# Performance work log

Measured on AMD Instinct MI355X. Metric: run time of the kernel, lower is better.

Reference implementation:

```python
import jax, jax.numpy as jnp
import numpy as np
from jax import lax

# Module constants (from init_kwargs)
B, C = 2, 64            # batch, in_channel
H, W, D = 64, 64, 64    # size
GROUPS = 2


def setup_inputs() -> dict:
    key = jax.random.key(0)
    ks = jax.random.split(key, 4)
    x = jax.random.normal(ks[0], (B, H * W * D, C), dtype=jnp.float32)
    # TransverseConv: Conv3d(2, W*2, (H,3,3), pad (0,1,1)) -> weight (O,I,kD,kH,kW)
    w_t = jax.random.normal(ks[1], (W * GROUPS, GROUPS, H, 3, 3), dtype=jnp.float32) * 0.02
    b_t = jnp.zeros((W * GROUPS,), jnp.float32)
    # CoronalConv: Conv3d(2, W*2, (3,3,D), pad (1,1,0))
    w_c = jax.random.normal(ks[2], (W * GROUPS, GROUPS, 3, 3, D), dtype=jnp.float32) * 0.02
    b_c = jnp.zeros((W * GROUPS,), jnp.float32)
    # map: Conv3d(2C, C, 1) stored as dense (C, 2C)
    w_map = jax.random.normal(ks[3], (C, 2 * C), dtype=jnp.float32) * 0.02
    b_map = jnp.zeros((C,), jnp.float32)
    return {"x": x, "w_t": w_t, "b_t": b_t, "w_c": w_c, "b_c": b_c,
            "w_map": w_map, "b_map": b_map}


def _forward(x, w_t, b_t, w_c, b_c, w_map, b_map):
    Bx, N, Cx = x.shape
    xg = x.transpose(0, 2, 1).reshape(Bx, Cx, H, W, D)   # (B,C,H,W,D)
    shortcut = xg
    xr = xg.reshape(Bx * Cx // GROUPS, GROUPS, H, W, D)
    dn = ('NCDHW', 'OIDHW', 'NCDHW')
    # Transverse: kernel spans full H -> output (B*C/2, 2W, 1, W, D)
    tans = lax.conv_general_dilated(xr, w_t, (1, 1, 1), [(0, 0), (1, 1), (1, 1)],
                                    dimension_numbers=dn)
    tans = tans + b_t[None, :, None, None, None]
    tans = tans.reshape(Bx, Cx, W, W, D)                 # (B,C,W,W,D)
    # Coronal: kernel spans full D -> output (B*C/2, 2W, H, W, 1)
    cor = lax.conv_general_dilated(xr, w_c, (1, 1, 1), [(1, 1), (1, 1), (0, 0)],
                                   dimension_numbers=dn)
    cor = cor + b_c[None, :, None, None, None]
    cor = cor.reshape(Bx, Cx, W, H, W)                   # (B,C,W,H,W)
    t1 = tans.transpose(0, 1, 3, 2, 4)                   # (B,C,W,W,D)
    c1 = cor.transpose(0, 1, 4, 3, 2)                    # (B,C,W,H,W)
    f = jnp.matmul(c1, t1).transpose(0, 1, 3, 2, 4)      # (B,C,H,W,D)
    attn = jnp.matmul(cor, tans).transpose(0, 1, 3, 2, 4)  # (B,C,H,W,D)
    cat = jnp.concatenate([shortcut * f, attn], axis=1)  # (B,2C,H,W,D)
    mapped = jnp.einsum('bkhwd,ck->bchwd', cat, w_map) + b_map[None, :, None, None, None]
    out = jax.nn.gelu(mapped, approximate=False)         # torch nn.GELU = exact erf
    return out.reshape(Bx, Cx, -1).transpose(0, 2, 1)    # (B,N,C)


def reference(x, w_t, b_t, w_c, b_c, w_map, b_map):
    return _forward(x, w_t, b_t, w_c, b_c, w_map, b_map)
```

## Files before the change

### kernel.cpp

```cpp
#include <hip/hip_runtime.h>
#include <hip/hip_bf16.h>
#include <math.h>

#define HWD 262144

typedef __attribute__((ext_vector_type(8))) short bf16x8;
typedef __attribute__((ext_vector_type(16))) float f32x16;

__device__ inline unsigned short bfu(float f) {
    __hip_bfloat16 h = __float2bfloat16(f);
    return *reinterpret_cast<unsigned short*>(&h);
}

__global__ void k_prep(const float* __restrict__ w_t, const float* __restrict__ w_c,
                       const float* __restrict__ w_map,
                       __hip_bfloat16* __restrict__ A_t, __hip_bfloat16* __restrict__ A_c,
                       __hip_bfloat16* __restrict__ Wb) {
    int i = blockIdx.x * 256 + threadIdx.x;
    if (i < 147456) {
        int kk = i & 15, oc = (i >> 4) & 127, ks = i >> 11;
        int z4 = ks & 3, kq = ks >> 2;
        int g = kq / 9, tap = kq - 9 * g;
        int z = z4 * 16 + kk;
        A_t[i] = __float2bfloat16(w_t[((oc * 2 + g) * 64 + z) * 9 + tap]);
        A_c[i] = __float2bfloat16(w_c[((oc * 2 + g) * 9 + tap) * 64 + z]);
    }
    if (i < 8192) {
        Wb[i] = __float2bfloat16(w_map[i]);
    }
}

__device__ inline void pack_row_bf16(__hip_bfloat16* dst, const float* src) {
    unsigned short u[16];
#pragma unroll
    for (int j = 0; j < 16; ++j) u[j] = bfu(src[j]);
    uint4* q = reinterpret_cast<uint4*>(dst);
    q[0] = *reinterpret_cast<const uint4*>(&u[0]);
    q[1] = *reinterpret_cast<const uint4*>(&u[8]);
}

__global__ void k_trans_c(const float* __restrict__ x, __hip_bfloat16* __restrict__ Xc) {
    __shared__ unsigned short tile[256][68];
    int b = blockIdx.y;
    long n0 = (long)blockIdx.x * 256;
    int t = threadIdx.x;
    const float4* xp4 = (const float4*)(x + ((long)b * HWD + n0) * 64);
#pragma unroll
    for (int i = 0; i < 16; ++i) {
        int f4i = i * 256 + t;
        float4 v = xp4[f4i];
        int nl = f4i >> 4, c4 = (f4i & 15) * 4;
        ushort4 u;
        u.x = bfu(v.x); u.y = bfu(v.y); u.z = bfu(v.z); u.w = bfu(v.w);
        *(ushort4*)&tile[nl][c4] = u;
    }
    __syncthreads();
    int c = t >> 2, hwl = t & 3;
    int hw0 = blockIdx.x * 4;
    __hip_bfloat16* dst0 = Xc + (long)(b * 64 + c) * HWD + (long)(hw0 + hwl) * 16;
#pragma unroll
    for (int z4 = 0; z4 < 4; ++z4) {
        unsigned short u[16];
#pragma unroll
        for (int j = 0; j < 16; ++j) u[j] = tile[hwl * 64 + z4 * 16 + j][c];
        __hip_bfloat16* dst = dst0 + z4 * 65536;
        *(uint4*)dst = *(const uint4*)&u[0];
        *(uint4*)(dst + 8) = *(const uint4*)&u[8];
    }
}

__global__ void k_trans_t(const float* __restrict__ x, __hip_bfloat16* __restrict__ Xt) {
    __shared__ unsigned short tile[256][68];
    int b = blockIdx.y;
    int wd0 = blockIdx.x * 4;
    int t = threadIdx.x;
    const float* xb = x + (long)b * HWD * 64 + (long)wd0 * 64;
#pragma unroll
    for (int i = 0; i < 16; ++i) {
        int idx = i * 256 + t;
        int h = idx >> 6, f = idx & 63;
        float4 v = *(const float4*)(xb + (long)h * 262144 + f * 4);
        int wdl = f >> 4, c4 = (f & 15) * 4;
        ushort4 u;
        u.x = bfu(v.x); u.y = bfu(v.y); u.z = bfu(v.z); u.w = bfu(v.w);
        *(ushort4*)&tile[wdl * 64 + h][c4] = u;
    }
    __syncthreads();
    int c = t >> 2, wdl = t & 3;
    __hip_bfloat16* dst0 = Xt + (long)(b * 64 + c) * HWD + (long)(wd0 + wdl) * 16;
#pragma unroll
    for (int z4 = 0; z4 < 4; ++z4) {
        unsigned short u[16];
#pragma unroll
        for (int j = 0; j < 16; ++j) u[j] = tile[wdl * 64 + z4 * 16 + j][c];
        __hip_bfloat16* dst = dst0 + z4 * 65536;
        *(uint4*)dst = *(const uint4*)&u[0];
        *(uint4*)(dst + 8) = *(const uint4*)&u[8];
    }
}

__global__ __launch_bounds__(256, 3) void k_conv_mfma(
        const __hip_bfloat16* __restrict__ X, const __hip_bfloat16* __restrict__ Aglob,
        const float* __restrict__ bias, float* __restrict__ Out) {
    int L = blockIdx.x;
    int grp = (L & 7) * 8 + ((L >> 3) >> 5);
    int pt = (L >> 3) & 31;
    int b = grp >> 5, ch = grp & 31;
    int p0 = pt * 2;
    const short* Xg = (const short*)(X + ((long)(b * 64 + 2 * ch)) * HWD);
    const short* Ag = (const short*)Aglob;
    int t = threadIdx.x;
    int lane = t & 63, wv = t >> 6;
    int O0 = (wv >> 1) * 64;
    int N0 = (wv & 1) * 64;
    int lrow = lane & 31, lq = lane >> 5;

    __shared__ __align__(16) short Bsm[2][4][2][1024];

    f32x16 acc00 = {0}, acc01 = {0}, acc10 = {0}, acc11 = {0};

    int srow = t >> 1, shalf = t & 1;
    int spr = srow >> 6, sq = srow & 63;
    const uint4 zero4 = {0u, 0u, 0u, 0u};
    uint4 ld0, ld1, ld2, ld3;

    auto stage_load = [&](int kq) {
        int g = (kq >= 9) ? 1 : 0;
        int tap = kq - 9 * g;
        int r = tap / 3, s = tap - 3 * r;
        int pp = p0 + spr + r - 1, qq = sq + s - 1;
        bool ok = ((unsigned)pp < 64u) && ((unsigned)qq < 64u);
        const short* px = Xg + (long)g * HWD + (pp * 64 + qq) * 16 + shalf * 8;
        ld0 = ok ? *(const uint4*)(px)           : zero4;
        ld1 = ok ? *(const uint4*)(px + 65536)   : zero4;
        ld2 = ok ? *(const uint4*)(px + 131072)  : zero4;
        ld3 = ok ? *(const uint4*)(px + 196608)  : zero4;
    };
    auto stage_write = [&](int buf) {
        *(uint4*)&Bsm[buf][0][shalf][srow * 8] = ld0;
        *(uint4*)&Bsm[buf][1][shalf][srow * 8] = ld1;
        *(uint4*)&Bsm[buf][2][shalf][srow * 8] = ld2;
        *(uint4*)&Bsm[buf][3][shalf][srow * 8] = ld3;
    };

    stage_load(0);
    stage_write(0);
    __syncthreads();

    int buf = 0;
    for (int kq = 0; kq < 18; ++kq) {
        if (kq < 17) stage_load(kq + 1);
#pragma unroll
        for (int z4 = 0; z4 < 4; ++z4) {
            int ks = kq * 4 + z4;
            const short* Apk = Ag + ks * 2048 + (O0 + lrow) * 16 + lq * 8;
            uint4 a0u = *(const uint4*)(Apk);
            uint4 a1u = *(const uint4*)(Apk + 512);
            bf16x8 a0 = *(bf16x8*)&a0u;
            bf16x8 a1 = *(bf16x8*)&a1u;
            bf16x8 b0 = *(const bf16x8*)&Bsm[buf][z4][lq][(N0 + lrow) * 8];
            bf16x8 b1 = *(const bf16x8*)&Bsm[buf][z4][lq][(N0 + 32 + lrow) * 8];
            acc00 = __builtin_amdgcn_mfma_f32_32x32x16_bf16(a0, b0, acc00, 0, 0, 0);
            acc01 = __builtin_amdgcn_mfma_f32_32x32x16_bf16(a0, b1, acc01, 0, 0, 0);
            acc10 = __builtin_amdgcn_mfma_f32_32x32x16_bf16(a1, b0, acc10, 0, 0, 0);
            acc11 = __builtin_amdgcn_mfma_f32_32x32x16_bf16(a1, b1, acc11, 0, 0, 0);
        }
        if (kq < 17) {
            stage_write(buf ^ 1);
            __syncthreads();
            buf ^= 1;
        }
    }

    long base0 = ((long)(b * 64 + 2 * ch)) * HWD + (long)p0 * 64;
    int n0l = N0 + lrow, n1l = N0 + 32 + lrow;
    long noff0 = (long)(n0l >> 6) * 64 + (n0l & 63);
    long noff1 = (long)(n1l >> 6) * 64 + (n1l & 63);
#pragma unroll
    for (int reg = 0; reg < 16; ++reg) {
        int row = (reg & 3) + 8 * (reg >> 2) + 4 * lq;
        int oc0 = O0 + row, oc1 = O0 + 32 + row;
        long cb0 = base0 + (long)(oc0 >> 6) * HWD + (long)(oc0 & 63) * 4096;
        long cb1 = base0 + (long)(oc1 >> 6) * HWD + (long)(oc1 & 63) * 4096;
        float bs0 = bias[oc0], bs1 = bias[oc1];
        Out[cb0 + noff0] = acc00[reg] + bs0;
        Out[cb0 + noff1] = acc01[reg] + bs0;
        Out[cb1 + noff0] = acc10[reg] + bs1;
        Out[cb1 + noff1] = acc11[reg] + bs1;
    }
}

__global__ __launch_bounds__(128) void k_attn(const float* __restrict__ Cc,
        const float* __restrict__ T, __hip_bfloat16* __restrict__ At) {
    __shared__ float As[64][65];
    __shared__ float Bs[64][64];
    int bc = blockIdx.x >> 6, w2 = blockIdx.x & 63;
    const float4* Ap4 = (const float4*)(Cc + ((long)bc * 64 + w2) * 4096);
    const float4* Bp4 = (const float4*)(T + ((long)bc * 64 + w2) * 4096);
    int t = threadIdx.x;
#pragma unroll
    for (int i = 0; i < 8; ++i) {
        int f = i * 128 + t;
        int r = f >> 4, q4 = (f & 15) * 4;
        float4 v = Ap4[f];
        As[r][q4 + 0] = v.x; As[r][q4 + 1] = v.y; As[r][q4 + 2] = v.z; As[r][q4 + 3] = v.w;
        float4 w = Bp4[f];
        *(float4*)&Bs[r][q4] = w;
    }
    __syncthreads();
    int h2 = t >> 2, dg = (t & 3) * 16;
    f32x16 acc0 = {0}, acc1 = {0};
    for (int k = 0; k < 64; ++k) {
        float a0 = As[h2][k];
        float a1 = As[h2 + 32][k];
        const float* br = &Bs[k][dg];
#pragma unroll
        for (int i = 0; i < 16; ++i) {
            acc0[i] = fmaf(a0, br[i], acc0[i]);
            acc1[i] = fmaf(a1, br[i], acc1[i]);
        }
    }
    float tmp[16];
    __hip_bfloat16* Ab = At + (long)bc * HWD + (long)h2 * 4096 + w2 * 64 + dg;
#pragma unroll
    for (int i = 0; i < 16; ++i) tmp[i] = acc0[i];
    pack_row_bf16(Ab, tmp);
#pragma unroll
    for (int i = 0; i < 16; ++i) tmp[i] = acc1[i];
    pack_row_bf16(Ab + 32L * 4096, tmp);
}

__global__ __launch_bounds__(512, 4) void k_f(const float* __restrict__ Cc,
        const float* __restrict__ T, __hip_bfloat16* __restrict__ F) {
    __shared__ float As[16][64][8];
    __shared__ float Bs[16][8][68];
    int L = blockIdx.x;
    int xcd = L & 7, j = L >> 3;
    int bc = xcd * 16 + (j >> 3), wt = j & 7;
    const float* Ab = Cc + (long)bc * HWD + wt * 8;
    const float* Bb = T + (long)bc * HWD + wt * 8 * 64;
    int t = threadIdx.x;
    int w = t & 7, h = t >> 3;
    f32x16 acc0 = {0}, acc1 = {0}, acc2 = {0}, acc3 = {0};

    for (int w2c = 0; w2c < 4; ++w2c) {
        __syncthreads();
#pragma unroll
        for (int i = 0; i < 4; ++i) {
            int f = i * 512 + t;
            int half = f & 1, hh = (f >> 1) & 63, kk = f >> 7;
            float4 v = *(const float4*)(Ab + (long)(w2c * 16 + kk) * 4096 + hh * 64 + half * 4);
            *(float4*)&As[kk][hh][half * 4] = v;
        }
#pragma unroll
        for (int i = 0; i < 4; ++i) {
            int f = i * 512 + t;
            int d4 = f & 15, ww = (f >> 4) & 7, kk = f >> 7;
            float4 v = *(const float4*)(Bb + (long)(w2c * 16 + kk) * 4096 + ww * 64 + d4 * 4);
            *(float4*)&Bs[kk][ww][d4 * 4] = v;
        }
        __syncthreads();
        for (int kk = 0; kk < 16; ++kk) {
            float a = As[kk][h][w];
            const float* br = &Bs[kk][w][0];
#pragma unroll
            for (int i = 0; i < 16; ++i) {
                acc0[i] = fmaf(a, br[i], acc0[i]);
                acc1[i] = fmaf(a, br[16 + i], acc1[i]);
                acc2[i] = fmaf(a, br[32 + i], acc2[i]);
                acc3[i] = fmaf(a, br[48 + i], acc3[i]);
            }
        }
    }
    __hip_bfloat16* Fp = F + (long)bc * HWD + (long)h * 4096 + (wt * 8 + w) * 64;
    float tmp[16];
#pragma unroll
    for (int i = 0; i < 16; ++i) tmp[i] = acc0[i];
    pack_row_bf16(Fp, tmp);
#pragma unroll
    for (int i = 0; i < 16; ++i) tmp[i] = acc1[i];
    pack_row_bf16(Fp + 16, tmp);
#pragma unroll
    for (int i = 0; i < 16; ++i) tmp[i] = acc2[i];
    pack_row_bf16(Fp + 32, tmp);
#pragma unroll
    for (int i = 0; i < 16; ++i) tmp[i] = acc3[i];
    pack_row_bf16(Fp + 48, tmp);
}

__global__ __launch_bounds__(256, 4) void k_map(const float* __restrict__ x,
        const __hip_bfloat16* __restrict__ F, const __hip_bfloat16* __restrict__ At,
        const __hip_bfloat16* __restrict__ Wb, const float* __restrict__ b_map,
        float* __restrict__ out) {
    __shared__ float xs[16][257];
    __shared__ __hip_bfloat16 fa[16][264];
    __shared__ short Pl[256][24];
    __shared__ short Wt[64][136];

    int t = threadIdx.x;
    long n0 = (long)blockIdx.x * 256;
    int b = (int)(n0 >> 18);
    long nn0 = n0 & (HWD - 1);
    const float* xblk = x + n0 * 64;
    const __hip_bfloat16* Fb = F + (long)b * 64 * HWD + nn0;
    const __hip_bfloat16* Ab = At + (long)b * 64 * HWD + nn0;

#pragma unroll
    for (int i = 0; i < 4; ++i) {
        int e = i * 256 + t;
        int c = e >> 4, kk = (e & 15) * 8;
        *(uint4*)&Wt[c][kk] = *(const uint4*)((const short*)Wb + c * 128 + kk);
    }

    int lane = t & 63, wv = t >> 6;
    int lrow = lane & 31, lhalf = lane >> 5;
    f32x16 acc00 = {0}, acc01 = {0}, acc10 = {0}, acc11 = {0};

    for (int kc = 0; kc < 8; ++kc) {
        __syncthreads();
        if (kc < 4) {
#pragma unroll
            for (int i2 = 0; i2 < 4; ++i2) {
                int f = i2 * 256 + t;
                int nr = f >> 2, j4 = (f & 3) * 4;
                float4 v = *(const float4*)(xblk + nr * 64 + kc * 16 + j4);
                xs[j4 + 0][nr] = v.x;
                xs[j4 + 1][nr] = v.y;
                xs[j4 + 2][nr] = v.z;
                xs[j4 + 3][nr] = v.w;
            }
#pragma unroll
            for (int it = 0; it < 2; ++it) {
                int idx = it * 256 + t;
                int row = idx >> 5, seg = idx & 31;
                *(uint4*)&fa[row][seg * 8] =
                    *(const uint4*)(Fb + (long)(kc * 16 + row) * HWD + seg * 8);
            }
        } else {
#pragma unroll
            for (int it = 0; it < 2; ++it) {
                int idx = it * 256 + t;
                int row = idx >> 5, seg = idx & 31;
                *(uint4*)&fa[row][seg * 8] =
                    *(const uint4*)(Ab + (long)((kc - 4) * 16 + row) * HWD + seg * 8);
            }
        }
        __syncthreads();
        unsigned short pv[16];
        if (kc < 4) {
#pragma unroll
            for (int k2 = 0; k2 < 16; ++k2) {
                float p = xs[k2][t] * __bfloat162float(fa[k2][t]);
                pv[k2] = bfu(p);
            }
        } else {
#pragma unroll
            for (int k2 = 0; k2 < 16; ++k2)
                pv[k2] = *reinterpret_cast<const unsigned short*>(&fa[k2][t]);
        }
        *(uint4*)&Pl[t][0] = *(uint4*)&pv[0];
        *(uint4*)&Pl[t][8] = *(uint4*)&pv[8];
        __syncthreads();
        bf16x8 a0 = *(const bf16x8*)&Pl[wv * 64 + lrow][lhalf * 8];
        bf16x8 a1 = *(const bf16x8*)&Pl[wv * 64 + 32 + lrow][lhalf * 8];
        bf16x8 b0 = *(const bf16x8*)&Wt[lrow][kc * 16 + lhalf * 8];
        bf16x8 b1 = *(const bf16x8*)&Wt[32 + lrow][kc * 16 + lhalf * 8];
        acc00 = __builtin_amdgcn_mfma_f32_32x32x16_bf16(a0, b0, acc00, 0, 0, 0);
        acc01 = __builtin_amdgcn_mfma_f32_32x32x16_bf16(a0, b1, acc01, 0, 0, 0);
        acc10 = __builtin_amdgcn_mfma_f32_32x32x16_bf16(a1, b0, acc10, 0, 0, 0);
        acc11 = __builtin_amdgcn_mfma_f32_32x32x16_bf16(a1, b1, acc11, 0, 0, 0);
    }

    float bs0 = b_map[lrow];
    float bs1 = b_map[32 + lrow];
    const float inv_sqrt2 = 0.70710678118654752440f;
    float* ob = out + (n0 + wv * 64) * 64;
#pragma unroll
    for (int reg = 0; reg < 16; ++reg) {
        int nrow = (reg & 3) + 8 * (reg >> 2) + 4 * lhalf;
        float v00 = acc00[reg] + bs0;
        float v01 = acc01[reg] + bs1;
        float v10 = acc10[reg] + bs0;
        float v11 = acc11[reg] + bs1;
        v00 = 0.5f * v00 * (1.f + erff(v00 * inv_sqrt2));
        v01 = 0.5f * v01 * (1.f + erff(v01 * inv_sqrt2));
        v10 = 0.5f * v10 * (1.f + erff(v10 * inv_sqrt2));
        v11 = 0.5f * v11 * (1.f + erff(v11 * inv_sqrt2));
        ob[(long)nrow * 64 + lrow] = v00;
        ob[(long)nrow * 64 + 32 + lrow] = v01;
        ob[(long)(32 + nrow) * 64 + lrow] = v10;
        ob[(long)(32 + nrow) * 64 + 32 + lrow] = v11;
    }
}

extern "C" void kernel_launch(void* const* d_in, const int* in_sizes, int n_in,
                              void* d_out, int out_size, void* d_ws, size_t ws_size,
                              hipStream_t stream) {
    const float* x     = (const float*)d_in[0];
    const float* w_t   = (const float*)d_in[1];
    const float* b_t   = (const float*)d_in[2];
    const float* w_c   = (const float*)d_in[3];
    const float* b_c   = (const float*)d_in[4];
    const float* w_map = (const float*)d_in[5];
    const float* b_map = (const float*)d_in[6];
    float* out = (float*)d_out;
    float* ws = (float*)d_ws;

    __hip_bfloat16* Xc = (__hip_bfloat16*)ws;
    __hip_bfloat16* Xt = (__hip_bfloat16*)(ws + 16777216L);
    float* T = ws + 33554432L;
    float* Cc = out;
    __hip_bfloat16* A_t = (__hip_bfloat16*)(ws + 67108864L);
    __hip_bfloat16* A_c = (__hip_bfloat16*)(ws + 67182592L);
    __hip_bfloat16* Wb = (__hip_bfloat16*)(ws + 67256320L);
    __hip_bfloat16* At_bf = Xc;
    __hip_bfloat16* F_bf = Xt;

    hipLaunchKernelGGL(k_prep, dim3(576), dim3(256), 0, stream, w_t, w_c, w_map, A_t, A_c, Wb);
    hipLaunchKernelGGL(k_trans_c, dim3(1024, 2), dim3(256), 0, stream, x, Xc);
    hipLaunchKernelGGL(k_trans_t, dim3(1024, 2), dim3(256), 0, stream, x, Xt);
    hipLaunchKernelGGL(k_conv_mfma, dim3(2048), dim3(256), 0, stream, Xt, A_t, b_t, T);
    hipLaunchKernelGGL(k_conv_mfma, dim3(2048), dim3(256), 0, stream, Xc, A_c, b_c, Cc);
    hipLaunchKernelGGL(k_attn, dim3(8192), dim3(128), 0, stream, Cc, T, At_bf);
    hipLaunchKernelGGL(k_f, dim3(1024), dim3(512), 0, stream, Cc, T, F_bf);
    hipLaunchKernelGGL(k_map, dim3(2048), dim3(256), 0, stream, x, F_bf, At_bf, Wb, b_map, out);
}
```

Measured before the change: 780.9 us.

## Replace LDS staging in k_map with lane shuffles and register weights; register-block k_f

In k_map, the elementwise product tile is no longer written to shared memory and re-read as MFMA A operands. The operands are now assembled with cross-lane shuffles, which removes an LDS round trip and a barrier per k-chunk. The map weights are preloaded into registers instead of being staged in LDS. k_f is halved to 256 threads, each computing two output rows for more register reuse of the B tile, at the cost of higher register pressure and lower occupancy.

```diff
diff --git a/kernel.cpp b/kernel.cpp
--- a/kernel.cpp
+++ b/kernel.cpp
@@ -230,7 +230,7 @@
     pack_row_bf16(Ab + 32L * 4096, tmp);
 }
 
-__global__ __launch_bounds__(512, 4) void k_f(const float* __restrict__ Cc,
+__global__ __launch_bounds__(256, 2) void k_f(const float* __restrict__ Cc,
         const float* __restrict__ T, __hip_bfloat16* __restrict__ F) {
     __shared__ float As[16][64][8];
     __shared__ float Bs[16][8][68];
@@ -240,62 +240,79 @@
     const float* Ab = Cc + (long)bc * HWD + wt * 8;
     const float* Bb = T + (long)bc * HWD + wt * 8 * 64;
     int t = threadIdx.x;
-    int w = t & 7, h = t >> 3;
-    f32x16 acc0 = {0}, acc1 = {0}, acc2 = {0}, acc3 = {0};
+    int w = t & 7, h2 = t >> 3;
+    f32x16 p00 = {0}, p01 = {0}, p02 = {0}, p03 = {0};
+    f32x16 p10 = {0}, p11 = {0}, p12 = {0}, p13 = {0};
 
     for (int w2c = 0; w2c < 4; ++w2c) {
         __syncthreads();
 #pragma unroll
-        for (int i = 0; i < 4; ++i) {
-            int f = i * 512 + t;
+        for (int i = 0; i < 8; ++i) {
+            int f = i * 256 + t;
             int half = f & 1, hh = (f >> 1) & 63, kk = f >> 7;
             float4 v = *(const float4*)(Ab + (long)(w2c * 16 + kk) * 4096 + hh * 64 + half * 4);
             *(float4*)&As[kk][hh][half * 4] = v;
         }
 #pragma unroll
-        for (int i = 0; i < 4; ++i) {
-            int f = i * 512 + t;
+        for (int i = 0; i < 8; ++i) {
+            int f = i * 256 + t;
             int d4 = f & 15, ww = (f >> 4) & 7, kk = f >> 7;
             float4 v = *(const float4*)(Bb + (long)(w2c * 16 + kk) * 4096 + ww * 64 + d4 * 4);
             *(float4*)&Bs[kk][ww][d4 * 4] = v;
         }
         __syncthreads();
         for (int kk = 0; kk < 16; ++kk) {
-            float a = As[kk][h][w];
+            float a0 = As[kk][h2][w];
+            float a1 = As[kk][h2 + 32][w];
             const float* br = &Bs[kk][w][0];
 #pragma unroll
             for (int i = 0; i < 16; ++i) {
-                acc0[i] = fmaf(a, br[i], acc0[i]);
-                acc1[i] = fmaf(a, br[16 + i], acc1[i]);
-                acc2[i] = fmaf(a, br[32 + i], acc2[i]);
-                acc3[i] = fmaf(a, br[48 + i], acc3[i]);
+                p00[i] = fmaf(a0, br[i], p00[i]);
+                p01[i] = fmaf(a0, br[16 + i], p01[i]);
+                p02[i] = fmaf(a0, br[32 + i], p02[i]);
+                p03[i] = fmaf(a0, br[48 + i], p03[i]);
+                p10[i] = fmaf(a1, br[i], p10[i]);
+                p11[i] = fmaf(a1, br[16 + i], p11[i]);
+                p12[i] = fmaf(a1, br[32 + i], p12[i]);
+                p13[i] = fmaf(a1, br[48 + i], p13[i]);
             }
         }
     }
-    __hip_bfloat16* Fp = F + (long)bc * HWD + (long)h * 4096 + (wt * 8 + w) * 64;
+    __hip_bfloat16* Fp = F + (long)bc * HWD + (long)h2 * 4096 + (wt * 8 + w) * 64;
     float tmp[16];
 #pragma unroll
-    for (int i = 0; i < 16; ++i) tmp[i] = acc0[i];
+    for (int i = 0; i < 16; ++i) tmp[i] = p00[i];
     pack_row_bf16(Fp, tmp);
 #pragma unroll
-    for (int i = 0; i < 16; ++i) tmp[i] = acc1[i];
+    for (int i = 0; i < 16; ++i) tmp[i] = p01[i];
     pack_row_bf16(Fp + 16, tmp);
 #pragma unroll
-    for (int i = 0; i < 16; ++i) tmp[i] = acc2[i];
+    for (int i = 0; i < 16; ++i) tmp[i] = p02[i];
     pack_row_bf16(Fp + 32, tmp);
 #pragma unroll
-    for (int i = 0; i < 16; ++i) tmp[i] = acc3[i];
+    for (int i = 0; i < 16; ++i) tmp[i] = p03[i];
     pack_row_bf16(Fp + 48, tmp);
-}
-
-__global__ __launch_bounds__(256, 4) void k_map(const float* __restrict__ x,
+    __hip_bfloat16* Fq = Fp + 32L * 4096;
+#pragma unroll
+    for (int i = 0; i < 16; ++i) tmp[i] = p10[i];
+    pack_row_bf16(Fq, tmp);
+#pragma unroll
+    for (int i = 0; i < 16; ++i) tmp[i] = p11[i];
+    pack_row_bf16(Fq + 16, tmp);
+#pragma unroll
+    for (int i = 0; i < 16; ++i) tmp[i] = p12[i];
+    pack_row_bf16(Fq + 32, tmp);
+#pragma unroll
+    for (int i = 0; i < 16; ++i) tmp[i] = p13[i];
+    pack_row_bf16(Fq + 48, tmp);
+}
+
+__global__ __launch_bounds__(256, 2) void k_map(const float* __restrict__ x,
         const __hip_bfloat16* __restrict__ F, const __hip_bfloat16* __restrict__ At,
         const __hip_bfloat16* __restrict__ Wb, const float* __restrict__ b_map,
         float* __restrict__ out) {
     __shared__ float xs[16][257];
     __shared__ __hip_bfloat16 fa[16][264];
-    __shared__ short Pl[256][24];
-    __shared__ short Wt[64][136];
 
     int t = threadIdx.x;
     long n0 = (long)blockIdx.x * 256;
@@ -305,17 +322,22 @@
     const __hip_bfloat16* Fb = F + (long)b * 64 * HWD + nn0;
     const __hip_bfloat16* Ab = At + (long)b * 64 * HWD + nn0;
 
-#pragma unroll
-    for (int i = 0; i < 4; ++i) {
-        int e = i * 256 + t;
-        int c = e >> 4, kk = (e & 15) * 8;
-        *(uint4*)&Wt[c][kk] = *(const uint4*)((const short*)Wb + c * 128 + kk);
-    }
-
     int lane = t & 63, wv = t >> 6;
     int lrow = lane & 31, lhalf = lane >> 5;
+
+    const short* Wp = (const short*)Wb;
+    bf16x8 wb0[8], wb1[8];
+#pragma unroll
+    for (int kc = 0; kc < 8; ++kc) {
+        uint4 u0 = *(const uint4*)(Wp + lrow * 128 + kc * 16 + lhalf * 8);
+        uint4 u1 = *(const uint4*)(Wp + (32 + lrow) * 128 + kc * 16 + lhalf * 8);
+        wb0[kc] = *(bf16x8*)&u0;
+        wb1[kc] = *(bf16x8*)&u1;
+    }
+
     f32x16 acc00 = {0}, acc01 = {0}, acc10 = {0}, acc11 = {0};
 
+#pragma unroll
     for (int kc = 0; kc < 8; ++kc) {
         __syncthreads();
         if (kc < 4) {
@@ -358,17 +380,31 @@
             for (int k2 = 0; k2 < 16; ++k2)
                 pv[k2] = *reinterpret_cast<const unsigned short*>(&fa[k2][t]);
         }
-        *(uint4*)&Pl[t][0] = *(uint4*)&pv[0];
-        *(uint4*)&Pl[t][8] = *(uint4*)&pv[8];
-        __syncthreads();
-        bf16x8 a0 = *(const bf16x8*)&Pl[wv * 64 + lrow][lhalf * 8];
-        bf16x8 a1 = *(const bf16x8*)&Pl[wv * 64 + 32 + lrow][lhalf * 8];
-        bf16x8 b0 = *(const bf16x8*)&Wt[lrow][kc * 16 + lhalf * 8];
-        bf16x8 b1 = *(const bf16x8*)&Wt[32 + lrow][kc * 16 + lhalf * 8];
-        acc00 = __builtin_amdgcn_mfma_f32_32x32x16_bf16(a0, b0, acc00, 0, 0, 0);
-        acc01 = __builtin_amdgcn_mfma_f32_32x32x16_bf16(a0, b1, acc01, 0, 0, 0);
-        acc10 = __builtin_amdgcn_mfma_f32_32x32x16_bf16(a1, b0, acc10, 0, 0, 0);
-        acc11 = __builtin_amdgcn_mfma_f32_32x32x16_bf16(a1, b1, acc11, 0, 0, 0);
+        unsigned lo0 = (unsigned)pv[0]  | ((unsigned)pv[1]  << 16);
+        unsigned lo1 = (unsigned)pv[2]  | ((unsigned)pv[3]  << 16);
+        unsigned lo2 = (unsigned)pv[4]  | ((unsigned)pv[5]  << 16);
+        unsigned lo3 = (unsigned)pv[6]  | ((unsigned)pv[7]  << 16);
+        unsigned hi0 = (unsigned)pv[8]  | ((unsigned)pv[9]  << 16);
+        unsigned hi1 = (unsigned)pv[10] | ((unsigned)pv[11] << 16);
+        unsigned hi2 = (unsigned)pv[12] | ((unsigned)pv[13] << 16);
+        unsigned hi3 = (unsigned)pv[14] | ((unsigned)pv[15] << 16);
+        int sl0 = lane & 31, sl1 = lane | 32;
+        bool lowh = lane < 32;
+        unsigned s00 = __shfl(hi0, sl0), s01 = __shfl(hi1, sl0);
+        unsigned s02 = __shfl(hi2, sl0), s03 = __shfl(hi3, sl0);
+        unsigned r00 = __shfl(lo0, sl1), r01 = __shfl(lo1, sl1);
+        unsigned r02 = __shfl(lo2, sl1), r03 = __shfl(lo3, sl1);
+        uint4 ua0, ua1;
+        ua0.x = lowh ? lo0 : s00; ua0.y = lowh ? lo1 : s01;
+        ua0.z = lowh ? lo2 : s02; ua0.w = lowh ? lo3 : s03;
+        ua1.x = lowh ? r00 : hi0; ua1.y = lowh ? r01 : hi1;
+        ua1.z = lowh ? r02 : hi2; ua1.w = lowh ? r03 : hi3;
+        bf16x8 a0 = *(bf16x8*)&ua0;
+        bf16x8 a1 = *(bf16x8*)&ua1;
+        acc00 = __builtin_amdgcn_mfma_f32_32x32x16_bf16(a0, wb0[kc], acc00, 0, 0, 0);
+        acc01 = __builtin_amdgcn_mfma_f32_32x32x16_bf16(a0, wb1[kc], acc01, 0, 0, 0);
+        acc10 = __builtin_amdgcn_mfma_f32_32x32x16_bf16(a1, wb0[kc], acc10, 0, 0, 0);
+        acc11 = __builtin_amdgcn_mfma_f32_32x32x16_bf16(a1, wb1[kc], acc11, 0, 0, 0);
     }
 
     float bs0 = b_map[lrow];
@@ -422,6 +458,6 @@
     hipLaunchKernelGGL(k_conv_mfma, dim3(2048), dim3(256), 0, stream, Xt, A_t, b_t, T);
     hipLaunchKernelGGL(k_conv_mfma, dim3(2048), dim3(256), 0, stream, Xc, A_c, b_c, Cc);
     hipLaunchKernelGGL(k_attn, dim3(8192), dim3(128), 0, stream, Cc, T, At_bf);
-    hipLaunchKernelGGL(k_f, dim3(1024), dim3(512), 0, stream, Cc, T, F_bf);
+    hipLaunchKernelGGL(k_f, dim3(1024), dim3(256), 0, stream, Cc, T, F_bf);
     hipLaunchKernelGGL(k_map, dim3(2048), dim3(256), 0, stream, x, F_bf, At_bf, Wb, b_map, out);
 }
```

Result: faster. 762.6 us (-2.3%).
